# Performance work log

Measured on AMD Instinct MI355X. Metric: run time of the kernel, lower is better.

## Reference

```python
import jax, jax.numpy as jnp
import numpy as np
from jax import lax

D_MODEL, D_INNER, D_STATE, D_CONV, DT_RANK = 128, 256, 16, 4, 8
BATCH, SEQ = 8, 4096


def setup_inputs() -> dict:
    key = jax.random.key(0)
    ks = jax.random.split(key, 13)
    g = lambda k, shape, fan: (jax.random.normal(k, shape, jnp.float32) / np.sqrt(fan)).astype(jnp.float32)
    inp = {
        "s": jax.random.normal(ks[0], (BATCH, SEQ, D_MODEL), jnp.float32),
        "in_proj_w": g(ks[1], (2 * D_INNER, D_MODEL), D_MODEL),
        "conv_w": g(ks[2], (D_INNER, 1, D_CONV), D_CONV),
        "conv_b": jnp.zeros((D_INNER,), jnp.float32),
        "x_proj_w": g(ks[3], (DT_RANK + 2 * D_STATE, D_INNER), D_INNER),
        "dt_proj_w": g(ks[4], (D_INNER, DT_RANK), DT_RANK),
        "dt_proj_b": jax.random.uniform(ks[5], (D_INNER,), jnp.float32, -4.0, -2.0),  # softplus(b) small, like mamba dt init
        "A_log": jnp.log(jnp.broadcast_to(jnp.arange(1, D_STATE + 1, dtype=jnp.float32), (D_INNER, D_STATE))),
        "D_skip": jnp.ones((D_INNER,), jnp.float32),
        "out_proj_w": g(ks[6], (D_MODEL, D_INNER), D_INNER),
        "ln_gamma": jnp.ones((D_MODEL,), jnp.float32),
        "ln_beta": jnp.zeros((D_MODEL,), jnp.float32),
        "fc_w": g(ks[7], (D_MODEL, D_MODEL), D_MODEL),
    }
    return inp


def _mamba(s, in_proj_w, conv_w, conv_b, x_proj_w, dt_proj_w, dt_proj_b, A_log, D_skip, out_proj_w):
    B, L, _ = s.shape
    xz = jnp.einsum("bld,ed->ble", s, in_proj_w)           # [B,L,2*D_INNER]
    x, z = jnp.split(xz, 2, axis=-1)                        # each [B,L,D_INNER]
    # causal depthwise conv1d
    xc = jnp.transpose(x, (0, 2, 1))                        # [B,D_INNER,L]
    xc = jnp.pad(xc, ((0, 0), (0, 0), (D_CONV - 1, 0)))
    xc = lax.conv_general_dilated(xc, conv_w, (1,), "VALID",
                                  dimension_numbers=("NCH", "OIH", "NCH"),
                                  feature_group_count=D_INNER)
    x = jax.nn.silu(jnp.transpose(xc + conv_b[None, :, None], (0, 2, 1)))  # [B,L,D_INNER]
    # input-dependent dt, B, C
    x_dbl = jnp.einsum("bld,ed->ble", x, x_proj_w)
    dt = x_dbl[..., :DT_RANK]
    Bc = x_dbl[..., DT_RANK:DT_RANK + D_STATE]              # [B,L,D_STATE]
    Cc = x_dbl[..., DT_RANK + D_STATE:]                     # [B,L,D_STATE]
    dt = jax.nn.softplus(jnp.einsum("blr,dr->bld", dt, dt_proj_w) + dt_proj_b)  # [B,L,D_INNER]
    A = -jnp.exp(A_log)                                     # [D_INNER,D_STATE]

    def step(h, inp):
        dt_t, b_t, c_t, u_t = inp                           # [B,Di],[B,Ds],[B,Ds],[B,Di]
        dA = jnp.exp(dt_t[:, :, None] * A)                  # [B,Di,Ds]
        dBu = (dt_t * u_t)[:, :, None] * b_t[:, None, :]
        h = dA * h + dBu
        y = jnp.einsum("bds,bs->bd", h, c_t)
        return h, y

    h0 = jnp.zeros((B, D_INNER, D_STATE), x.dtype)
    xs = (jnp.swapaxes(dt, 0, 1), jnp.swapaxes(Bc, 0, 1), jnp.swapaxes(Cc, 0, 1), jnp.swapaxes(x, 0, 1))
    _, ys = lax.scan(step, h0, xs)                          # ys: [L,B,D_INNER]
    y = jnp.swapaxes(ys, 0, 1) + x * D_skip
    y = y * jax.nn.silu(z)
    return jnp.einsum("bld,od->blo", y, out_proj_w)         # [B,L,D_MODEL]


def reference(s, in_proj_w, conv_w, conv_b, x_proj_w, dt_proj_w, dt_proj_b, A_log, D_skip, out_proj_w, ln_gamma, ln_beta, fc_w):
    h = _mamba(s, in_proj_w, conv_w, conv_b, x_proj_w, dt_proj_w, dt_proj_b, A_log, D_skip, out_proj_w)
    mu = jnp.mean(h, axis=-1, keepdims=True)
    var = jnp.mean(jnp.square(h - mu), axis=-1, keepdims=True)
    hn = (h - mu) * lax.rsqrt(var + 1e-5) * ln_gamma + ln_beta
    return jax.nn.relu(jnp.einsum("bld,od->blo", hn, fc_w))
```

## Files before the change

kernel.cpp:

```cpp
#include <hip/hip_runtime.h>
#include <math.h>

#define B_ 8
#define L_ 4096
#define DM 128
#define DI 256
#define DSN 16
#define RK 8
#define M_ (B_*L_)
#define NC 128
#define CH 32

typedef __attribute__((ext_vector_type(8))) short bfrag;
typedef __attribute__((ext_vector_type(4))) float ffrag;
typedef __attribute__((ext_vector_type(2))) float f32x2;

__device__ __forceinline__ float silu_f(float x) {
  return x * __builtin_amdgcn_rcpf(1.f + __expf(-x));
}
__device__ __forceinline__ float softplus_f(float x) {
  return (x > 20.f) ? x : __logf(1.f + __expf(x));
}

__device__ __forceinline__ unsigned short f2bf(float f) {
  unsigned int u = __builtin_bit_cast(unsigned int, f);
  unsigned int r = (u + 0x7FFFu + ((u >> 16) & 1u)) >> 16;
  return (unsigned short)r;
}
__device__ __forceinline__ unsigned int f2bf2(float lo, float hi) {
  return (unsigned int)f2bf(lo) | ((unsigned int)f2bf(hi) << 16);
}
__device__ __forceinline__ float bf2f(unsigned int us) {
  return __builtin_bit_cast(float, us << 16);
}

__global__ __launch_bounds__(256)
void gemm_bf16_in(const float* __restrict__ A, const float* __restrict__ W,
                  unsigned short* __restrict__ xb, unsigned short* __restrict__ zsb) {
  __shared__ unsigned short As[64 * 136];
  __shared__ unsigned short Ws[64 * 136];
  __shared__ unsigned short Os[64 * 72];
  const int t = threadIdx.x;
  const int m0 = blockIdx.y << 6;
  const int half = blockIdx.x;
  unsigned short* __restrict__ outp = half ? zsb : xb;
  const float* __restrict__ Wbase = W + (half << 8) * 128;
  for (int i = t; i < 64 * 32; i += 256) {
    int row = i >> 5, c4 = i & 31;
    float4 av = *(const float4*)&A[(m0 + row) * 128 + (c4 << 2)];
    uint2 ap = {f2bf2(av.x, av.y), f2bf2(av.z, av.w)};
    *(uint2*)&As[row * 136 + (c4 << 2)] = ap;
  }
  float4 wr[8];
#pragma unroll
  for (int k = 0; k < 8; ++k) {
    int i = t + (k << 8);
    int row = i >> 5, c4 = i & 31;
    wr[k] = *(const float4*)&Wbase[row * 128 + (c4 << 2)];
  }
#pragma unroll
  for (int k = 0; k < 8; ++k) {
    int i = t + (k << 8);
    int row = i >> 5, c4 = i & 31;
    uint2 wp = {f2bf2(wr[k].x, wr[k].y), f2bf2(wr[k].z, wr[k].w)};
    *(uint2*)&Ws[row * 136 + (c4 << 2)] = wp;
  }
  __syncthreads();
  const int w = t >> 6, l = t & 63, q = l >> 4, col = l & 15;
  for (int jt = 0; jt < 4; ++jt) {
    if (jt < 3) {
#pragma unroll
      for (int k = 0; k < 8; ++k) {
        int i = t + (k << 8);
        int row = i >> 5, c4 = i & 31;
        wr[k] = *(const float4*)&Wbase[(((jt + 1) << 6) + row) * 128 + (c4 << 2)];
      }
    }
    ffrag acc[4] = {{0.f,0.f,0.f,0.f},{0.f,0.f,0.f,0.f},{0.f,0.f,0.f,0.f},{0.f,0.f,0.f,0.f}};
#pragma unroll
    for (int s = 0; s < 4; ++s) {
      int k0 = s * 32 + q * 8;
      bfrag af = *(const bfrag*)&As[((w << 4) + col) * 136 + k0];
#pragma unroll
      for (int nt = 0; nt < 4; ++nt) {
        bfrag bf_ = *(const bfrag*)&Ws[((nt << 4) + col) * 136 + k0];
        acc[nt] = __builtin_amdgcn_mfma_f32_16x16x32_bf16(af, bf_, acc[nt], 0, 0, 0);
      }
    }
    __syncthreads();
#pragma unroll
    for (int nt = 0; nt < 4; ++nt)
#pragma unroll
      for (int i = 0; i < 4; ++i) {
        int ml = (w << 4) + (q << 2) + i;
        float v = acc[nt][i];
        if (half) v = silu_f(v);
        Os[ml * 72 + (nt << 4) + col] = f2bf(v);
      }
    if (jt < 3) {
#pragma unroll
      for (int k = 0; k < 8; ++k) {
        int i = t + (k << 8);
        int row = i >> 5, c4 = i & 31;
        uint2 wp = {f2bf2(wr[k].x, wr[k].y), f2bf2(wr[k].z, wr[k].w)};
        *(uint2*)&Ws[row * 136 + (c4 << 2)] = wp;
      }
    }
    __syncthreads();
    {
      int r = t >> 2, c8 = (t & 3) << 3;
      int m = m0 + r;
      *(uint4*)&outp[m * 256 + (jt << 6) + c8]      = *(const uint4*)&Os[r * 72 + c8];
      *(uint4*)&outp[m * 256 + (jt << 6) + 32 + c8] = *(const uint4*)&Os[r * 72 + 32 + c8];
    }
  }
}

__global__ __launch_bounds__(256)
void gemm_bf16_out(const unsigned short* __restrict__ Ab, const float* __restrict__ W,
                   unsigned short* __restrict__ C) {
  __shared__ unsigned short As[64 * 264];
  __shared__ unsigned short Ws[64 * 264];
  const int t = threadIdx.x;
  const int m0 = blockIdx.y << 6, n0 = blockIdx.x << 6;
  for (int i = t; i < 64 * 32; i += 256) {
    int row = i >> 5, c8 = i & 31;
    uint4 av = *(const uint4*)&Ab[(m0 + row) * 256 + (c8 << 3)];
    *(uint4*)&As[row * 264 + (c8 << 3)] = av;
  }
  for (int i = t; i < 64 * 64; i += 256) {
    int row = i >> 6, c4 = i & 63;
    float4 wv = *(const float4*)&W[(n0 + row) * 256 + (c4 << 2)];
    uint2 wp = {f2bf2(wv.x, wv.y), f2bf2(wv.z, wv.w)};
    *(uint2*)&Ws[row * 264 + (c4 << 2)] = wp;
  }
  __syncthreads();
  const int w = t >> 6, l = t & 63, q = l >> 4, col = l & 15;
  ffrag acc[4] = {{0.f,0.f,0.f,0.f},{0.f,0.f,0.f,0.f},{0.f,0.f,0.f,0.f},{0.f,0.f,0.f,0.f}};
#pragma unroll
  for (int s = 0; s < 8; ++s) {
    int k0 = s * 32 + q * 8;
    bfrag af = *(const bfrag*)&As[((w << 4) + col) * 264 + k0];
#pragma unroll
    for (int nt = 0; nt < 4; ++nt) {
      bfrag bf_ = *(const bfrag*)&Ws[((nt << 4) + col) * 264 + k0];
      acc[nt] = __builtin_amdgcn_mfma_f32_16x16x32_bf16(af, bf_, acc[nt], 0, 0, 0);
    }
  }
#pragma unroll
  for (int nt = 0; nt < 4; ++nt)
#pragma unroll
    for (int i = 0; i < 4; ++i) {
      int ml = (w << 4) + (q << 2) + i;
      C[(m0 + ml) * 128 + n0 + (nt << 4) + col] = f2bf(acc[nt][i]);
    }
}

__global__ __launch_bounds__(512)
void xproj_dtproj(const unsigned short* __restrict__ xb, const float* __restrict__ xw,
                  const float* __restrict__ dtw, const float* __restrict__ dtpb,
                  const float* __restrict__ cw, const float* __restrict__ cb,
                  float* __restrict__ Bb, float* __restrict__ Cb,
                  unsigned int* __restrict__ udt) {
  __shared__ unsigned short ua[64 * 264];
  __shared__ unsigned short wb[48 * 264];
  __shared__ float dtr_s[64 * 12];
  const int t = threadIdx.x;
  const int p0 = blockIdx.x << 6;
  {
    const int k = t & 255, half = t >> 8;
    const int pstart = half << 5;
    const int base = p0 + pstart;
    const int lb = base & (L_ - 1);
    const float w0 = cw[k*4], w1 = cw[k*4+1], w2 = cw[k*4+2], w3 = cw[k*4+3];
    const float bias = cb[k];
    float x0 = (lb >= 3) ? bf2f((unsigned int)xb[(base - 3) * 256 + k]) : 0.f;
    float x1 = (lb >= 2) ? bf2f((unsigned int)xb[(base - 2) * 256 + k]) : 0.f;
    float x2 = (lb >= 1) ? bf2f((unsigned int)xb[(base - 1) * 256 + k]) : 0.f;
#pragma unroll 8
    for (int it = 0; it < 32; ++it) {
      float x3 = bf2f((unsigned int)xb[(base + it) * 256 + k]);
      float u = silu_f(fmaf(w0, x0, fmaf(w1, x1, fmaf(w2, x2, fmaf(w3, x3, bias)))));
      ua[(pstart + it) * 264 + k] = f2bf(u);
      x0 = x1; x1 = x2; x2 = x3;
    }
  }
  for (int i = t; i < 40 * 256; i += 512) {
    int n = i >> 8, k = i & 255;
    wb[n * 264 + k] = f2bf(xw[i]);
  }
  for (int i = t; i < 8 * 264; i += 512) wb[40 * 264 + i] = 0;
  __syncthreads();
  const int w = t >> 6, l = t & 63, q = l >> 4, col = l & 15;
  for (int tile = w; tile < 12; tile += 8) {
    const int mt = tile & 3, nt = tile >> 2;
    ffrag acc = {0.f, 0.f, 0.f, 0.f};
#pragma unroll
    for (int s = 0; s < 8; ++s) {
      int k0 = s * 32 + q * 8;
      bfrag af = *(const bfrag*)&ua[((mt << 4) + col) * 264 + k0];
      bfrag bf_ = *(const bfrag*)&wb[((nt << 4) + col) * 264 + k0];
      acc = __builtin_amdgcn_mfma_f32_16x16x32_bf16(af, bf_, acc, 0, 0, 0);
    }
#pragma unroll
    for (int i = 0; i < 4; ++i) {
      int ml = (mt << 4) + (q << 2) + i;
      int m = p0 + ml;
      if (nt == 0) {
        if (col < 8) dtr_s[ml * 12 + col] = acc[i];
        else         Bb[m * 16 + (col - 8)] = acc[i];
      } else if (nt == 1) {
        if (col < 8) Bb[m * 16 + 8 + col] = acc[i];
        else         Cb[m * 16 + (col - 8)] = acc[i];
      } else {
        if (col < 8) Cb[m * 16 + 8 + col] = acc[i];
      }
    }
  }
  __syncthreads();
  {
    const int d = t & 255, half = t >> 8;
    const int pstart = half << 5;
    float w8[8];
    *(float4*)&w8[0] = *(const float4*)&dtw[d * 8];
    *(float4*)&w8[4] = *(const float4*)&dtw[d * 8 + 4];
    const float bias = dtpb[d];
#pragma unroll 4
    for (int pp = pstart; pp < pstart + 32; ++pp) {
      float r0[8];
      *(float4*)&r0[0] = *(const float4*)&dtr_s[pp * 12];
      *(float4*)&r0[4] = *(const float4*)&dtr_s[pp * 12 + 4];
      float a2 = bias;
#pragma unroll
      for (int r2 = 0; r2 < 8; ++r2) a2 = fmaf(r0[r2], w8[r2], a2);
      float sp = softplus_f(a2);
      udt[(p0 + pp) * 256 + d] =
          (unsigned int)ua[pp * 264 + d] | ((unsigned int)f2bf(sp) << 16);
    }
  }
}

__global__ __launch_bounds__(512, 4)
void scan_phase1(const unsigned int* __restrict__ udt,
                 const float* __restrict__ Bb, const float* __restrict__ alog,
                 unsigned short* __restrict__ cP, unsigned short* __restrict__ cHe) {
  __shared__ float Bs[CH * 16];
  const int bc = blockIdx.x;
  const int b = bc >> 7, c = bc & (NC - 1);
  const int t = threadIdx.x;
  const int l = t & 63, w = t >> 6;
  const int d = (w << 5) + (l & 31);
  const int sh = l >> 5;
  const int soff = sh << 3;
  const int base = b * L_ + c * CH;
  if (t < CH * 4) ((float4*)Bs)[t] = *(const float4*)&Bb[base * 16 + (t << 2)];
  float a[8];
  bool okl = true;
#pragma unroll
  for (int j = 0; j < 8; ++j) {
    a[j] = -__expf(alog[d * 16 + soff + j]);
    float tgt = (float)(soff + j + 1);
    okl = okl && (fabsf(a[j] + tgt) <= 1e-3f * tgt);
  }
  const bool fast = (bool)__all((int)okl);
  f32x2 h2[4] = {{0.f,0.f},{0.f,0.f},{0.f,0.f},{0.f,0.f}};
  float sdt = 0.f;
  unsigned int wv0 = udt[base * 256 + d];
  unsigned int wv1 = udt[(base + 1) * 256 + d];
  __syncthreads();
#pragma unroll 4
  for (int ll = 0; ll < CH; ++ll) {
    const int m2 = base + ((ll + 2 < CH) ? ll + 2 : CH - 1);
    unsigned int wv2 = udt[m2 * 256 + d];
    float4 b0 = *(const float4*)&Bs[ll * 16 + soff];
    float4 b1 = *(const float4*)&Bs[ll * 16 + soff + 4];
    float uv  = bf2f(wv0 & 0xFFFFu);
    float dtv = bf2f(wv0 >> 16);
    f32x2 B2[4] = {{b0.x,b0.y},{b0.z,b0.w},{b1.x,b1.y},{b1.z,b1.w}};
    float du = dtv * uv;
    sdt += dtv;
    if (fast) {
      float e1 = __expf(-dtv);
      float e2 = e1 * e1, e4 = e2 * e2, e8 = e4 * e4;
      float st = sh ? e8 * e1 : e1;
      f32x2 dA = {st, st * e1};
      f32x2 e22 = {e2, e2};
      f32x2 du2 = {du, du};
#pragma unroll
      for (int j = 0; j < 4; ++j) {
        h2[j] = dA * h2[j] + du2 * B2[j];
        dA = dA * e22;
      }
    } else {
#pragma unroll
      for (int j = 0; j < 8; ++j) {
        float dA = __expf(dtv * a[j]);
        h2[j >> 1][j & 1] = fmaf(dA, h2[j >> 1][j & 1], du * B2[j >> 1][j & 1]);
      }
    }
    wv0 = wv1; wv1 = wv2;
  }
#pragma unroll
  for (int j = 0; j < 8; ++j) {
    int o = (bc * 16 + soff + j) * 256 + d;
    cP[o]  = f2bf(__expf(a[j] * sdt));
    cHe[o] = f2bf(h2[j >> 1][j & 1]);
  }
}

__global__ __launch_bounds__(512)
void scan_combine(unsigned short* __restrict__ cP, const unsigned short* __restrict__ cHe) {
  __shared__ float segP[64 * 9], segH[64 * 9], segS[64 * 9];
  const int t = threadIdx.x;
  const int sdl = t & 63, seg = t >> 6;
  const int blk = blockIdx.x;
  const int b = blk >> 6, grp = blk & 63;
  const int sd = (grp << 6) + sdl;
  const int base = b * NC * 4096 + sd;
  float Pacc = 1.f, Hacc = 0.f;
#pragma unroll
  for (int i = 0; i < 16; ++i) {
    int idx = base + (seg * 16 + i) * 4096;
    float p = bf2f((unsigned int)cP[idx]);
    float he = bf2f((unsigned int)cHe[idx]);
    Hacc = fmaf(p, Hacc, he);
    Pacc *= p;
  }
  segP[sdl * 9 + seg] = Pacc;
  segH[sdl * 9 + seg] = Hacc;
  __syncthreads();
  if (t < 64) {
    float hs = 0.f;
#pragma unroll
    for (int s2 = 0; s2 < 8; ++s2) {
      segS[t * 9 + s2] = hs;
      hs = fmaf(segP[t * 9 + s2], hs, segH[t * 9 + s2]);
    }
  }
  __syncthreads();
  float hs = segS[sdl * 9 + seg];
#pragma unroll
  for (int i = 0; i < 16; ++i) {
    int idx = base + (seg * 16 + i) * 4096;
    float p = bf2f((unsigned int)cP[idx]);
    float he = bf2f((unsigned int)cHe[idx]);
    cP[idx] = f2bf(hs);
    hs = fmaf(p, hs, he);
  }
}

__global__ __launch_bounds__(512, 4)
void scan_phase3(const unsigned int* __restrict__ udt,
                 const float* __restrict__ Bb, const float* __restrict__ Cb,
                 const float* __restrict__ alog, const unsigned short* __restrict__ hst,
                 const float* __restrict__ dsk,
                 const unsigned short* __restrict__ zsb,
                 unsigned short* __restrict__ yb) {
  __shared__ float Bs[CH * 16];
  __shared__ float Cs[CH * 16];
  const int bc = blockIdx.x;
  const int b = bc >> 7, c = bc & (NC - 1);
  const int t = threadIdx.x;
  const int l = t & 63, w = t >> 6;
  const int d = (w << 5) + (l & 31);
  const int sh = l >> 5;
  const int soff = sh << 3;
  const int base = b * L_ + c * CH;
  if (t < CH * 4)            ((float4*)Bs)[t]            = *(const float4*)&Bb[base * 16 + (t << 2)];
  else if (t < CH * 8)       ((float4*)Cs)[t - CH * 4]   = *(const float4*)&Cb[base * 16 + ((t - CH * 4) << 2)];
  float a[8];
  bool okl = true;
#pragma unroll
  for (int j = 0; j < 8; ++j) {
    a[j] = -__expf(alog[d * 16 + soff + j]);
    float tgt = (float)(soff + j + 1);
    okl = okl && (fabsf(a[j] + tgt) <= 1e-3f * tgt);
  }
  const bool fast = (bool)__all((int)okl);
  const float dskv = dsk[d];
  f32x2 h2[4];
#pragma unroll
  for (int j = 0; j < 8; ++j)
    h2[j >> 1][j & 1] = bf2f((unsigned int)hst[(bc * 16 + soff + j) * 256 + d]);
  unsigned int wv0 = udt[base * 256 + d];
  unsigned int wv1 = udt[(base + 1) * 256 + d];
  unsigned short zv0 = zsb[base * 256 + d];
  unsigned short zv1 = zsb[(base + 1) * 256 + d];
  __syncthreads();
#pragma unroll 4
  for (int ll = 0; ll < CH; ++ll) {
    const int m = base + ll;
    const int m2 = base + ((ll + 2 < CH) ? ll + 2 : CH - 1);
    unsigned int wv2 = udt[m2 * 256 + d];
    unsigned short zv2 = zsb[m2 * 256 + d];
    float4 b0 = *(const float4*)&Bs[ll * 16 + soff];
    float4 b1 = *(const float4*)&Bs[ll * 16 + soff + 4];
    float4 c0 = *(const float4*)&Cs[ll * 16 + soff];
    float4 c1 = *(const float4*)&Cs[ll * 16 + soff + 4];
    float uv  = bf2f(wv0 & 0xFFFFu);
    float dtv = bf2f(wv0 >> 16);
    f32x2 B2[4] = {{b0.x,b0.y},{b0.z,b0.w},{b1.x,b1.y},{b1.z,b1.w}};
    f32x2 C2[4] = {{c0.x,c0.y},{c0.z,c0.w},{c1.x,c1.y},{c1.z,c1.w}};
    float du = dtv * uv;
    f32x2 y2 = {0.f, 0.f};
    if (fast) {
      float e1 = __expf(-dtv);
      float e2 = e1 * e1, e4 = e2 * e2, e8 = e4 * e4;
      float st = sh ? e8 * e1 : e1;
      f32x2 dA = {st, st * e1};
      f32x2 e22 = {e2, e2};
      f32x2 du2 = {du, du};
#pragma unroll
      for (int j = 0; j < 4; ++j) {
        h2[j] = dA * h2[j] + du2 * B2[j];
        y2 = y2 + h2[j] * C2[j];
        dA = dA * e22;
      }
    } else {
#pragma unroll
      for (int j = 0; j < 8; ++j) {
        float dA = __expf(dtv * a[j]);
        float hh = fmaf(dA, h2[j >> 1][j & 1], du * B2[j >> 1][j & 1]);
        h2[j >> 1][j & 1] = hh;
        y2[j & 1] = fmaf(hh, C2[j >> 1][j & 1], y2[j & 1]);
      }
    }
    float y = y2.x + y2.y;
    y += __shfl_xor(y, 32);
    if (sh == 0) {
      float zs = bf2f((unsigned int)zv0);
      yb[m * 256 + d] = f2bf(fmaf(uv, dskv, y) * zs);
    }
    wv0 = wv1; wv1 = wv2; zv0 = zv1; zv1 = zv2;
  }
}

__global__ __launch_bounds__(256)
void ln_fc_mfma(const unsigned short* __restrict__ Hin, const float* __restrict__ gamma,
                const float* __restrict__ beta, const float* __restrict__ fcw,
                float* __restrict__ out) {
  __shared__ unsigned short hnb[64 * 136];
  __shared__ unsigned short wb[128 * 136];
  const int t = threadIdx.x;
  const int p0 = blockIdx.x << 6;
  {
    const int r = t >> 2, qd = t & 3;
    const unsigned short* hp = &Hin[(p0 + r) * 128 + (qd << 5)];
    float v[32];
#pragma unroll
    for (int j = 0; j < 4; ++j) {
      uint4 hv = *(const uint4*)&hp[j << 3];
      unsigned int hw[4] = {hv.x, hv.y, hv.z, hv.w};
#pragma unroll
      for (int k2 = 0; k2 < 4; ++k2) {
        v[(j << 3) + 2*k2]     = bf2f(hw[k2] & 0xFFFFu);
        v[(j << 3) + 2*k2 + 1] = bf2f(hw[k2] >> 16);
      }
    }
    float s1 = 0.f, s2 = 0.f;
#pragma unroll
    for (int j = 0; j < 32; ++j) { s1 += v[j]; s2 = fmaf(v[j], v[j], s2); }
    s1 += __shfl_xor(s1, 1); s2 += __shfl_xor(s2, 1);
    s1 += __shfl_xor(s1, 2); s2 += __shfl_xor(s2, 2);
    float mu = s1 * (1.f / DM);
    float var = s2 * (1.f / DM) - mu * mu;
    float rs = rsqrtf(var + 1e-5f);
    const float* gp = &gamma[qd << 5];
    const float* bp = &beta[qd << 5];
#pragma unroll
    for (int j = 0; j < 16; ++j) {
      float h0 = fmaf((v[2*j]   - mu) * rs, gp[2*j],   bp[2*j]);
      float h1 = fmaf((v[2*j+1] - mu) * rs, gp[2*j+1], bp[2*j+1]);
      *(unsigned int*)&hnb[r * 136 + (qd << 5) + 2*j] = f2bf2(h0, h1);
    }
  }
  for (int i = t; i < 128 * 32; i += 256) {
    int row = i >> 5, c4 = i & 31;
    float4 wv = *(const float4*)&fcw[row * 128 + (c4 << 2)];
    uint2 wp = {f2bf2(wv.x, wv.y), f2bf2(wv.z, wv.w)};
    *(uint2*)&wb[row * 136 + (c4 << 2)] = wp;
  }
  __syncthreads();
  const int w = t >> 6, l = t & 63, q = l >> 4, col = l & 15;
  ffrag acc[8] = {{0.f,0.f,0.f,0.f},{0.f,0.f,0.f,0.f},{0.f,0.f,0.f,0.f},{0.f,0.f,0.f,0.f},
                  {0.f,0.f,0.f,0.f},{0.f,0.f,0.f,0.f},{0.f,0.f,0.f,0.f},{0.f,0.f,0.f,0.f}};
#pragma unroll
  for (int s = 0; s < 4; ++s) {
    int k0 = s * 32 + q * 8;
    bfrag af = *(const bfrag*)&hnb[((w << 4) + col) * 136 + k0];
#pragma unroll
    for (int nt = 0; nt < 8; ++nt) {
      bfrag bf_ = *(const bfrag*)&wb[((nt << 4) + col) * 136 + k0];
      acc[nt] = __builtin_amdgcn_mfma_f32_16x16x32_bf16(af, bf_, acc[nt], 0, 0, 0);
    }
  }
#pragma unroll
  for (int nt = 0; nt < 8; ++nt)
#pragma unroll
    for (int i = 0; i < 4; ++i) {
      int ml = (w << 4) + (q << 2) + i;
      out[(p0 + ml) * 128 + (nt << 4) + col] = fmaxf(acc[nt][i], 0.f);
    }
}

extern "C" void kernel_launch(void* const* d_in, const int* in_sizes, int n_in,
                              void* d_out, int out_size, void* d_ws, size_t ws_size,
                              hipStream_t stream) {
  (void)in_sizes; (void)n_in; (void)out_size; (void)ws_size;
  const float* s    = (const float*)d_in[0];
  const float* w_in = (const float*)d_in[1];
  const float* cw   = (const float*)d_in[2];
  const float* cb   = (const float*)d_in[3];
  const float* xw   = (const float*)d_in[4];
  const float* dtw  = (const float*)d_in[5];
  const float* dtpb = (const float*)d_in[6];
  const float* alog = (const float*)d_in[7];
  const float* dsk  = (const float*)d_in[8];
  const float* ow   = (const float*)d_in[9];
  const float* gam  = (const float*)d_in[10];
  const float* bet  = (const float*)d_in[11];
  const float* fcw  = (const float*)d_in[12];
  float* out = (float*)d_out;
  float* ws  = (float*)d_ws;

  unsigned short* xb   = (unsigned short*)ws;
  unsigned short* zsb  = (unsigned short*)(ws + 4194304);
  unsigned int*   udt  = (unsigned int*)(ws + 8388608);
  float*          Bb   = ws + 16777216;
  float*          Cb   = ws + 17301504;
  unsigned short* cP   = (unsigned short*)(ws + 17825792);
  unsigned short* cHe  = (unsigned short*)(ws + 19922944);
  unsigned short* yb   = (unsigned short*)(ws + 22020096);
  unsigned short* hmid = (unsigned short*)(ws + 26214400);

  gemm_bf16_in<<<dim3(2, 512), 256, 0, stream>>>(s, w_in, xb, zsb);
  xproj_dtproj<<<512, 512, 0, stream>>>(xb, xw, dtw, dtpb, cw, cb, Bb, Cb, udt);
  scan_phase1<<<B_ * NC, 512, 0, stream>>>(udt, Bb, alog, cP, cHe);
  scan_combine<<<512, 512, 0, stream>>>(cP, cHe);
  scan_phase3<<<B_ * NC, 512, 0, stream>>>(udt, Bb, Cb, alog, cP, dsk, zsb, yb);
  gemm_bf16_out<<<dim3(2, 512), 256, 0, stream>>>(yb, ow, hmid);
  ln_fc_mfma<<<512, 256, 0, stream>>>(hmid, gam, bet, fcw, out);
}
```

Before: 207.9 us.

## Fuse out_proj GEMM with LayerNorm and fc GEMM into one kernel

Merges the output projection GEMM, LayerNorm and the fc GEMM with ReLU into a single kernel per 64-row tile. The intermediate hmid buffer and one kernel launch are removed. LayerNorm statistics are computed directly from the MFMA accumulators using lane shuffles. In exchange, each block computes both column halves of the out GEMM sequentially with fewer blocks and more LDS, which may reduce occupancy.

```diff
diff --git a/kernel.cpp b/kernel.cpp
--- a/kernel.cpp
+++ b/kernel.cpp
@@ -117,42 +117,99 @@
 }
 
 __global__ __launch_bounds__(256)
-void gemm_bf16_out(const unsigned short* __restrict__ Ab, const float* __restrict__ W,
-                   unsigned short* __restrict__ C) {
-  __shared__ unsigned short As[64 * 264];
-  __shared__ unsigned short Ws[64 * 264];
+void out_ln_fc(const unsigned short* __restrict__ Yb, const float* __restrict__ W,
+               const float* __restrict__ gamma, const float* __restrict__ beta,
+               const float* __restrict__ fcw, float* __restrict__ out) {
+  __shared__ unsigned short smA[64 * 264];
+  __shared__ unsigned short smB[128 * 136];
   const int t = threadIdx.x;
-  const int m0 = blockIdx.y << 6, n0 = blockIdx.x << 6;
+  const int m0 = blockIdx.x << 6;
   for (int i = t; i < 64 * 32; i += 256) {
     int row = i >> 5, c8 = i & 31;
-    uint4 av = *(const uint4*)&Ab[(m0 + row) * 256 + (c8 << 3)];
-    *(uint4*)&As[row * 264 + (c8 << 3)] = av;
-  }
-  for (int i = t; i < 64 * 64; i += 256) {
-    int row = i >> 6, c4 = i & 63;
-    float4 wv = *(const float4*)&W[(n0 + row) * 256 + (c4 << 2)];
+    uint4 av = *(const uint4*)&Yb[(m0 + row) * 256 + (c8 << 3)];
+    *(uint4*)&smA[row * 264 + (c8 << 3)] = av;
+  }
+  const int w = t >> 6, l = t & 63, q = l >> 4, col = l & 15;
+  ffrag acc[2][4];
+  for (int nt2 = 0; nt2 < 2; ++nt2) {
+    __syncthreads();
+    for (int i = t; i < 64 * 64; i += 256) {
+      int row = i >> 6, c4 = i & 63;
+      float4 wv = *(const float4*)&W[((nt2 << 6) + row) * 256 + (c4 << 2)];
+      uint2 wp = {f2bf2(wv.x, wv.y), f2bf2(wv.z, wv.w)};
+      *(uint2*)&smB[row * 264 + (c4 << 2)] = wp;
+    }
+    __syncthreads();
+#pragma unroll
+    for (int nt = 0; nt < 4; ++nt) acc[nt2][nt] = (ffrag){0.f, 0.f, 0.f, 0.f};
+#pragma unroll
+    for (int s = 0; s < 8; ++s) {
+      int k0 = s * 32 + q * 8;
+      bfrag af = *(const bfrag*)&smA[((w << 4) + col) * 264 + k0];
+#pragma unroll
+      for (int nt = 0; nt < 4; ++nt) {
+        bfrag bf_ = *(const bfrag*)&smB[((nt << 4) + col) * 264 + k0];
+        acc[nt2][nt] = __builtin_amdgcn_mfma_f32_16x16x32_bf16(af, bf_, acc[nt2][nt], 0, 0, 0);
+      }
+    }
+  }
+  float mu[4], rs[4];
+#pragma unroll
+  for (int i = 0; i < 4; ++i) {
+    float s1 = 0.f, s2 = 0.f;
+#pragma unroll
+    for (int nt2 = 0; nt2 < 2; ++nt2)
+#pragma unroll
+      for (int nt = 0; nt < 4; ++nt) {
+        float v = acc[nt2][nt][i];
+        s1 += v; s2 = fmaf(v, v, s2);
+      }
+    s1 += __shfl_xor(s1, 1); s2 += __shfl_xor(s2, 1);
+    s1 += __shfl_xor(s1, 2); s2 += __shfl_xor(s2, 2);
+    s1 += __shfl_xor(s1, 4); s2 += __shfl_xor(s2, 4);
+    s1 += __shfl_xor(s1, 8); s2 += __shfl_xor(s2, 8);
+    mu[i] = s1 * (1.f / DM);
+    float var = s2 * (1.f / DM) - mu[i] * mu[i];
+    rs[i] = rsqrtf(var + 1e-5f);
+  }
+  __syncthreads();
+#pragma unroll
+  for (int nt2 = 0; nt2 < 2; ++nt2)
+#pragma unroll
+    for (int nt = 0; nt < 4; ++nt) {
+      int n = (nt2 << 6) + (nt << 4) + col;
+      float g = gamma[n], be = beta[n];
+#pragma unroll
+      for (int i = 0; i < 4; ++i) {
+        int r = (w << 4) + (q << 2) + i;
+        smA[r * 136 + n] = f2bf(fmaf((acc[nt2][nt][i] - mu[i]) * rs[i], g, be));
+      }
+    }
+  for (int i = t; i < 128 * 32; i += 256) {
+    int row = i >> 5, c4 = i & 31;
+    float4 wv = *(const float4*)&fcw[row * 128 + (c4 << 2)];
     uint2 wp = {f2bf2(wv.x, wv.y), f2bf2(wv.z, wv.w)};
-    *(uint2*)&Ws[row * 264 + (c4 << 2)] = wp;
-  }
-  __syncthreads();
-  const int w = t >> 6, l = t & 63, q = l >> 4, col = l & 15;
-  ffrag acc[4] = {{0.f,0.f,0.f,0.f},{0.f,0.f,0.f,0.f},{0.f,0.f,0.f,0.f},{0.f,0.f,0.f,0.f}};
-#pragma unroll
-  for (int s = 0; s < 8; ++s) {
+    *(uint2*)&smB[row * 136 + (c4 << 2)] = wp;
+  }
+  __syncthreads();
+  ffrag a2[8] = {{0.f,0.f,0.f,0.f},{0.f,0.f,0.f,0.f},{0.f,0.f,0.f,0.f},{0.f,0.f,0.f,0.f},
+                 {0.f,0.f,0.f,0.f},{0.f,0.f,0.f,0.f},{0.f,0.f,0.f,0.f},{0.f,0.f,0.f,0.f}};
+#pragma unroll
+  for (int s = 0; s < 4; ++s) {
     int k0 = s * 32 + q * 8;
-    bfrag af = *(const bfrag*)&As[((w << 4) + col) * 264 + k0];
-#pragma unroll
-    for (int nt = 0; nt < 4; ++nt) {
-      bfrag bf_ = *(const bfrag*)&Ws[((nt << 4) + col) * 264 + k0];
-      acc[nt] = __builtin_amdgcn_mfma_f32_16x16x32_bf16(af, bf_, acc[nt], 0, 0, 0);
-    }
-  }
-#pragma unroll
-  for (int nt = 0; nt < 4; ++nt)
+    bfrag af = *(const bfrag*)&smA[((w << 4) + col) * 136 + k0];
+#pragma unroll
+    for (int nt = 0; nt < 8; ++nt) {
+      bfrag bf_ = *(const bfrag*)&smB[((nt << 4) + col) * 136 + k0];
+      a2[nt] = __builtin_amdgcn_mfma_f32_16x16x32_bf16(af, bf_, a2[nt], 0, 0, 0);
+    }
+  }
+#pragma unroll
+  for (int nt = 0; nt < 8; ++nt)
 #pragma unroll
     for (int i = 0; i < 4; ++i) {
       int ml = (w << 4) + (q << 2) + i;
-      C[(m0 + ml) * 128 + n0 + (nt << 4) + col] = f2bf(acc[nt][i]);
+      out[(m0 + ml) * 128 + (nt << 4) + col] = fmaxf(a2[nt][i], 0.f);
     }
 }
 
@@ -435,74 +492,6 @@
   }
 }
 
-__global__ __launch_bounds__(256)
-void ln_fc_mfma(const unsigned short* __restrict__ Hin, const float* __restrict__ gamma,
-                const float* __restrict__ beta, const float* __restrict__ fcw,
-                float* __restrict__ out) {
-  __shared__ unsigned short hnb[64 * 136];
-  __shared__ unsigned short wb[128 * 136];
-  const int t = threadIdx.x;
-  const int p0 = blockIdx.x << 6;
-  {
-    const int r = t >> 2, qd = t & 3;
-    const unsigned short* hp = &Hin[(p0 + r) * 128 + (qd << 5)];
-    float v[32];
-#pragma unroll
-    for (int j = 0; j < 4; ++j) {
-      uint4 hv = *(const uint4*)&hp[j << 3];
-      unsigned int hw[4] = {hv.x, hv.y, hv.z, hv.w};
-#pragma unroll
-      for (int k2 = 0; k2 < 4; ++k2) {
-        v[(j << 3) + 2*k2]     = bf2f(hw[k2] & 0xFFFFu);
-        v[(j << 3) + 2*k2 + 1] = bf2f(hw[k2] >> 16);
-      }
-    }
-    float s1 = 0.f, s2 = 0.f;
-#pragma unroll
-    for (int j = 0; j < 32; ++j) { s1 += v[j]; s2 = fmaf(v[j], v[j], s2); }
-    s1 += __shfl_xor(s1, 1); s2 += __shfl_xor(s2, 1);
-    s1 += __shfl_xor(s1, 2); s2 += __shfl_xor(s2, 2);
-    float mu = s1 * (1.f / DM);
-    float var = s2 * (1.f / DM) - mu * mu;
-    float rs = rsqrtf(var + 1e-5f);
-    const float* gp = &gamma[qd << 5];
-    const float* bp = &beta[qd << 5];
-#pragma unroll
-    for (int j = 0; j < 16; ++j) {
-      float h0 = fmaf((v[2*j]   - mu) * rs, gp[2*j],   bp[2*j]);
-      float h1 = fmaf((v[2*j+1] - mu) * rs, gp[2*j+1], bp[2*j+1]);
-      *(unsigned int*)&hnb[r * 136 + (qd << 5) + 2*j] = f2bf2(h0, h1);
-    }
-  }
-  for (int i = t; i < 128 * 32; i += 256) {
-    int row = i >> 5, c4 = i & 31;
-    float4 wv = *(const float4*)&fcw[row * 128 + (c4 << 2)];
-    uint2 wp = {f2bf2(wv.x, wv.y), f2bf2(wv.z, wv.w)};
-    *(uint2*)&wb[row * 136 + (c4 << 2)] = wp;
-  }
-  __syncthreads();
-  const int w = t >> 6, l = t & 63, q = l >> 4, col = l & 15;
-  ffrag acc[8] = {{0.f,0.f,0.f,0.f},{0.f,0.f,0.f,0.f},{0.f,0.f,0.f,0.f},{0.f,0.f,0.f,0.f},
-                  {0.f,0.f,0.f,0.f},{0.f,0.f,0.f,0.f},{0.f,0.f,0.f,0.f},{0.f,0.f,0.f,0.f}};
-#pragma unroll
-  for (int s = 0; s < 4; ++s) {
-    int k0 = s * 32 + q * 8;
-    bfrag af = *(const bfrag*)&hnb[((w << 4) + col) * 136 + k0];
-#pragma unroll
-    for (int nt = 0; nt < 8; ++nt) {
-      bfrag bf_ = *(const bfrag*)&wb[((nt << 4) + col) * 136 + k0];
-      acc[nt] = __builtin_amdgcn_mfma_f32_16x16x32_bf16(af, bf_, acc[nt], 0, 0, 0);
-    }
-  }
-#pragma unroll
-  for (int nt = 0; nt < 8; ++nt)
-#pragma unroll
-    for (int i = 0; i < 4; ++i) {
-      int ml = (w << 4) + (q << 2) + i;
-      out[(p0 + ml) * 128 + (nt << 4) + col] = fmaxf(acc[nt][i], 0.f);
-    }
-}
-
 extern "C" void kernel_launch(void* const* d_in, const int* in_sizes, int n_in,
                               void* d_out, int out_size, void* d_ws, size_t ws_size,
                               hipStream_t stream) {
@@ -531,13 +520,11 @@
   unsigned short* cP   = (unsigned short*)(ws + 17825792);
   unsigned short* cHe  = (unsigned short*)(ws + 19922944);
   unsigned short* yb   = (unsigned short*)(ws + 22020096);
-  unsigned short* hmid = (unsigned short*)(ws + 26214400);
 
   gemm_bf16_in<<<dim3(2, 512), 256, 0, stream>>>(s, w_in, xb, zsb);
   xproj_dtproj<<<512, 512, 0, stream>>>(xb, xw, dtw, dtpb, cw, cb, Bb, Cb, udt);
   scan_phase1<<<B_ * NC, 512, 0, stream>>>(udt, Bb, alog, cP, cHe);
   scan_combine<<<512, 512, 0, stream>>>(cP, cHe);
   scan_phase3<<<B_ * NC, 512, 0, stream>>>(udt, Bb, Cb, alog, cP, dsk, zsb, yb);
-  gemm_bf16_out<<<dim3(2, 512), 256, 0, stream>>>(yb, ow, hmid);
-  ln_fc_mfma<<<512, 256, 0, stream>>>(hmid, gam, bet, fcw, out);
-}
+  out_ln_fc<<<512, 256, 0, stream>>>(yb, ow, gam, bet, fcw, out);
+}
```

Result: faster. 196.6 us (-5.4%).
